# Kernel tuning notes

Hardware: AMD Instinct MI355X
Metric: run time of the kernel (lower is better)

Reference implementation:

```python
import jax, jax.numpy as jnp
import numpy as np

V = 96103   # pegasus-xsum vocab
D = 1024    # d_model
H = 16      # heads
DH = D // H
F = 4096    # ffn
L = 2       # enc and dec layers (reduced from 16 for the reference)
S = 512     # source length
T = 80      # max_length
B = 4       # batch of sources
NS = 5      # num_return_sequences
BN = B * NS # decode streams
TOPK = 100
EOS = 1
MINLEN = 7
EMB_SCALE = float(np.sqrt(D))


def ln(x):
    m = jnp.mean(x, -1, keepdims=True)
    v = jnp.mean((x - m) ** 2, -1, keepdims=True)
    return (x - m) * jax.lax.rsqrt(v + 1e-5)


def setup_inputs() -> dict:
    key = jax.random.key(0)
    ks = jax.random.split(key, 16)
    g = lambda k, s: (jax.random.normal(k, s) * 0.02).astype(jnp.float32)
    return {
        "ids": jax.random.randint(ks[0], (B, S), 0, 96000).astype(jnp.int32),
        "mask": jnp.ones((B, S), jnp.int32),
        "E": g(ks[1], (V, D)),
        "pos_e": g(ks[2], (S, D)),
        "pos_d": g(ks[3], (T, D)),
        "enc_attn_in": g(ks[4], (L, D, 3 * D)),
        "enc_attn_out": g(ks[5], (L, D, D)),
        "enc_ffn1": g(ks[6], (L, D, F)),
        "enc_ffn2": g(ks[7], (L, F, D)),
        "dec_sa_in": g(ks[8], (L, D, 3 * D)),
        "dec_sa_out": g(ks[9], (L, D, D)),
        "dec_ca_q": g(ks[10], (L, D, D)),
        "dec_ca_kv": g(ks[11], (L, D, 2 * D)),
        "dec_ca_out": g(ks[12], (L, D, D)),
        "dec_ffn1": g(ks[13], (L, D, F)),
        "dec_ffn2": g(ks[14], (L, F, D)),
    }


def _generate(ids, mask, E, pos_e, pos_d, enc_attn_in, enc_attn_out, enc_ffn1,
              enc_ffn2, dec_sa_in, dec_sa_out, dec_ca_q, dec_ca_kv, dec_ca_out,
              dec_ffn1, dec_ffn2):
    inv = 1.0 / float(np.sqrt(DH))
    # ---------------- encoder ----------------
    x = E[ids] * EMB_SCALE + pos_e[None]                       # [B,S,D]
    bias = (1.0 - mask.astype(jnp.float32))[:, None, None, :] * -1e9  # [B,1,1,S]
    for l in range(L):
        h = ln(x)
        qkv = h @ enc_attn_in[l]
        q = qkv[..., :D].reshape(B, S, H, DH)
        k = qkv[..., D:2 * D].reshape(B, S, H, DH)
        v = qkv[..., 2 * D:].reshape(B, S, H, DH)
        sc = jnp.einsum('bqhd,bkhd->bhqk', q, k) * inv + bias
        a = jnp.einsum('bhqk,bkhd->bqhd', jax.nn.softmax(sc, -1), v).reshape(B, S, D)
        x = x + a @ enc_attn_out[l]
        h = ln(x)
        x = x + jax.nn.gelu(h @ enc_ffn1[l]) @ enc_ffn2[l]
    enc = ln(x)
    # expand to BN = B * num_return_sequences decode streams
    enc_r = jnp.repeat(enc, NS, axis=0)                        # [BN,S,D]
    bias_r = jnp.repeat(bias, NS, axis=0)[:, :, 0, :]          # [BN,1,S]
    # precompute cross-attn K/V per decoder layer
    ckv = jnp.einsum('bsd,lde->lbse', enc_r, dec_ca_kv)        # [L,BN,S,2D]
    cK = ckv[..., :D].reshape(L, BN, S, H, DH)
    cV = ckv[..., D:].reshape(L, BN, S, H, DH)

    key_base = jax.random.key(1234)
    cache_k0 = jnp.zeros((L, BN, T, H, DH), jnp.float32)
    cache_v0 = jnp.zeros((L, BN, T, H, DH), jnp.float32)

    def step(carry, t):
        ck, cv, prev = carry
        x = E[prev] * EMB_SCALE + pos_d[t]                     # [BN,D]
        for l in range(L):
            h = ln(x)
            qkv = h @ dec_sa_in[l]
            q = qkv[:, :D].reshape(BN, H, DH)
            k = qkv[:, D:2 * D].reshape(BN, H, DH)
            v = qkv[:, 2 * D:].reshape(BN, H, DH)
            ck = ck.at[l, :, t].set(k)
            cv = cv.at[l, :, t].set(v)
            sc = jnp.einsum('bhd,bkhd->bhk', q, ck[l]) * inv
            sc = sc + jnp.where(jnp.arange(T) <= t, 0.0, -1e9)
            a = jnp.einsum('bhk,bkhd->bhd', jax.nn.softmax(sc, -1), cv[l]).reshape(BN, D)
            x = x + a @ dec_sa_out[l]
            h = ln(x)
            q2 = (h @ dec_ca_q[l]).reshape(BN, H, DH)
            sc2 = jnp.einsum('bhd,bshd->bhs', q2, cK[l]) * inv + bias_r
            a2 = jnp.einsum('bhs,bshd->bhd', jax.nn.softmax(sc2, -1), cV[l]).reshape(BN, D)
            x = x + a2 @ dec_ca_out[l]
            h = ln(x)
            x = x + jax.nn.gelu(h @ dec_ffn1[l]) @ dec_ffn2[l]
        x = ln(x)
        logits = x @ E.T                                       # [BN,V]
        forbid = (t < MINLEN - 1) & (jnp.arange(V) == EOS)     # min_length: block EOS
        logits = jnp.where(forbid, -1e9, logits)
        topv, topi = jax.lax.top_k(logits, TOPK)               # top_k=100 sampling
        sel = jax.random.categorical(jax.random.fold_in(key_base, t), topv)
        tok = jnp.take_along_axis(topi, sel[:, None], 1)[:, 0]
        lp = jnp.take_along_axis(jax.nn.log_softmax(logits, -1), tok[:, None], 1)[:, 0]
        return (ck, cv, tok), (tok, lp)

    init = (cache_k0, cache_v0, jnp.zeros((BN,), jnp.int32))  # start token = pad(0)
    _, (toks, lps) = jax.lax.scan(step, init, jnp.arange(T))
    return toks.T, lps.T                                       # [BN,T] each


def reference(ids, mask, E, pos_e, pos_d, enc_attn_in, enc_attn_out, enc_ffn1,
              enc_ffn2, dec_sa_in, dec_sa_out, dec_ca_q, dec_ca_kv, dec_ca_out,
              dec_ffn1, dec_ffn2):
    toks, _ = _generate(ids, mask, E, pos_e, pos_d, enc_attn_in, enc_attn_out,
                        enc_ffn1, enc_ffn2, dec_sa_in, dec_sa_out, dec_ca_q,
                        dec_ca_kv, dec_ca_out, dec_ffn1, dec_ffn2)
    # matches the torch module: [batch, num_seq, max_len] token ids
    return toks.reshape(B, NS, T)
```

## Files before the change

kernel.cpp:

```cpp
#include <hip/hip_runtime.h>
#include <cstdint>
#include <cstddef>

#define DEV __device__ __forceinline__

constexpr int V  = 96103;
constexpr int VPAD = 96104;
constexpr int D  = 1024;
constexpr int H  = 16;
constexpr int DH = 64;
constexpr int F  = 4096;
constexpr int NL = 2;
constexpr int S  = 512;
constexpr int T  = 80;
constexpr int B  = 4;
constexpr int NS = 5;
constexpr int BN = 20;
constexpr int KTOP = 100;
constexpr int EOS = 1;
constexpr int LCOLS = 188;
constexpr int LGRID = (V + LCOLS - 1) / LCOLS;


DEV float gelu_f(float x) {
  float x3 = x * x * x;
  float inner = 0.7978845608028654f * (x + 0.044715f * x3);
  float tt = tanhf(inner);
  return x * (0.5f * (1.0f + tt));
}

DEV void tf2x32(unsigned k0, unsigned k1, unsigned& x0, unsigned& x1) {
  unsigned ks2 = k0 ^ k1 ^ 0x1BD11BDAu;
#define TFR(rr) { x0 += x1; x1 = (x1 << rr) | (x1 >> (32 - rr)); x1 ^= x0; }
  x0 += k0; x1 += k1;
  TFR(13) TFR(15) TFR(26) TFR(6)
  x0 += k1;  x1 += ks2 + 1u;
  TFR(17) TFR(29) TFR(16) TFR(24)
  x0 += ks2; x1 += k0 + 2u;
  TFR(13) TFR(15) TFR(26) TFR(6)
  x0 += k0;  x1 += k1 + 3u;
  TFR(17) TFR(29) TFR(16) TFR(24)
  x0 += k1;  x1 += ks2 + 4u;
  TFR(13) TFR(15) TFR(26) TFR(6)
  x0 += ks2; x1 += k0 + 5u;
#undef TFR
}

DEV unsigned long long sort_key(float v, unsigned idx) {
  unsigned bb = __float_as_uint(v);
  bb = (bb & 0x80000000u) ? ~bb : (bb | 0x80000000u);
  return ((unsigned long long)bb << 32) | (unsigned long long)(0xFFFFFFFFu - idx);
}

template<int NWAVE>
DEV void ln_to_lds(const float* __restrict__ x, float* xs, int tid) {
  int w = tid >> 6, lane = tid & 63;
  for (int m = w; m < BN; m += NWAVE) {
    float4 v[4];
    float sum = 0.0f;
#pragma unroll
    for (int j = 0; j < 4; ++j) {
      v[j] = *(const float4*)(x + m * D + j * 256 + lane * 4);
      sum += v[j].x + v[j].y + v[j].z + v[j].w;
    }
#pragma unroll
    for (int o = 32; o > 0; o >>= 1) sum += __shfl_xor(sum, o);
    float mean = sum * (1.0f / 1024.0f);
    float vs = 0.0f;
#pragma unroll
    for (int j = 0; j < 4; ++j) {
      float a = v[j].x - mean, b = v[j].y - mean, c = v[j].z - mean, d = v[j].w - mean;
      vs += a * a + b * b + c * c + d * d;
    }
#pragma unroll
    for (int o = 32; o > 0; o >>= 1) vs += __shfl_xor(vs, o);
    float rsig = 1.0f / sqrtf(vs * (1.0f / 1024.0f) + 1e-5f);
#pragma unroll
    for (int j = 0; j < 4; ++j) {
      float4 ov;
      ov.x = (v[j].x - mean) * rsig; ov.y = (v[j].y - mean) * rsig;
      ov.z = (v[j].z - mean) * rsig; ov.w = (v[j].w - mean) * rsig;
      *(float4*)(xs + m * D + j * 256 + lane * 4) = ov;
    }
  }
}

DEV void row_ln_stats(const float* __restrict__ xd, int bn, float* xrow,
                      float* wred, float& rstd, float& bco, int tid) {
  int w = tid >> 6, lane = tid & 63;
  float4 v = *(const float4*)(xd + (size_t)bn * D + w * 256 + lane * 4);
  *(float4*)(xrow + w * 256 + lane * 4) = v;
  float s = v.x + v.y + v.z + v.w;
#pragma unroll
  for (int o = 32; o > 0; o >>= 1) s += __shfl_xor(s, o);
  if (lane == 0) wred[w] = s;
  __syncthreads();
  float mean = (wred[0] + wred[1] + wred[2] + wred[3]) * (1.0f / 1024.0f);
  float a = v.x - mean, b = v.y - mean, c = v.z - mean, d = v.w - mean;
  float s2 = a * a + b * b + c * c + d * d;
#pragma unroll
  for (int o = 32; o > 0; o >>= 1) s2 += __shfl_xor(s2, o);
  if (lane == 0) wred[4 + w] = s2;
  __syncthreads();
  rstd = 1.0f / sqrtf((wred[4] + wred[5] + wred[6] + wred[7]) * (1.0f / 1024.0f) + 1e-5f);
  bco = -mean * rstd;
}


__global__ __launch_bounds__(256) void embed_enc(const int* __restrict__ ids,
                                                 const float* __restrict__ E,
                                                 const float* __restrict__ pos_e,
                                                 float* __restrict__ xe) {
  int row = blockIdx.x;
  int id = ids[row];
  const float* er = E + (size_t)id * D;
  const float* pr = pos_e + (size_t)(row % S) * D;
  float* xr = xe + (size_t)row * D;
  for (int j = threadIdx.x; j < D; j += 256)
    xr[j] = er[j] * 32.0f + pr[j];
}

__global__ __launch_bounds__(256) void embed_dec(const float* __restrict__ E,
                                                 const float* __restrict__ pos_d,
                                                 const int* __restrict__ toks,
                                                 float* __restrict__ xd, int t) {
  int bn = blockIdx.x;
  int prev = (t == 0) ? 0 : toks[bn * T + (t - 1)];
  const float* er = E + (size_t)prev * D;
  const float* pr = pos_d + (size_t)t * D;
  float* xr = xd + (size_t)bn * D;
  for (int j = threadIdx.x; j < D; j += 256)
    xr[j] = er[j] * 32.0f + pr[j];
}


__global__ __launch_bounds__(256) void ln_kernel(const float* __restrict__ x,
                                                 float* __restrict__ y) {
  __shared__ float red[256];
  __shared__ float sv[2];
  int tid = threadIdx.x;
  const float* xr = x + (size_t)blockIdx.x * D;
  float4 v = *(const float4*)(xr + tid * 4);
  red[tid] = v.x + v.y + v.z + v.w;
  __syncthreads();
  for (int k = 128; k > 0; k >>= 1) { if (tid < k) red[tid] += red[tid + k]; __syncthreads(); }
  if (tid == 0) sv[0] = red[0] * (1.0f / 1024.0f);
  __syncthreads();
  float m = sv[0];
  float dx = v.x - m, dy = v.y - m, dz = v.z - m, dw = v.w - m;
  red[tid] = dx * dx + dy * dy + dz * dz + dw * dw;
  __syncthreads();
  for (int k = 128; k > 0; k >>= 1) { if (tid < k) red[tid] += red[tid + k]; __syncthreads(); }
  if (tid == 0) sv[1] = 1.0f / sqrtf(red[0] * (1.0f / 1024.0f) + 1e-5f);
  __syncthreads();
  float r = sv[1];
  float* yr = y + (size_t)blockIdx.x * D;
  float4 o; o.x = dx * r; o.y = dy * r; o.z = dz * r; o.w = dw * r;
  *(float4*)(yr + tid * 4) = o;
}


template<int EPI>
__global__ __launch_bounds__(256) void gemm128(const float* __restrict__ A,
                                               const float* __restrict__ W,
                                               const float* X, float* C,
                                               int Kd, int Nd) {
  __shared__ __align__(16) float As[8][128];
  __shared__ __align__(16) float Bs[8][128];
  int tid = threadIdx.x;
  int n0 = blockIdx.x * 128, m0 = blockIdx.y * 128;
  int tx = tid & 15, ty = tid >> 4;
  int ar = tid >> 1, ac = (tid & 1) * 4;
  int br = tid >> 5, bc = (tid & 31) * 4;
  float acc[8][8] = {};
  for (int k0 = 0; k0 < Kd; k0 += 8) {
    float4 av = *(const float4*)(A + (size_t)(m0 + ar) * Kd + k0 + ac);
    float4 wv = *(const float4*)(W + (size_t)(k0 + br) * Nd + n0 + bc);
    __syncthreads();
    As[ac + 0][ar] = av.x; As[ac + 1][ar] = av.y;
    As[ac + 2][ar] = av.z; As[ac + 3][ar] = av.w;
    *(float4*)&Bs[br][bc] = wv;
    __syncthreads();
#pragma unroll
    for (int k = 0; k < 8; ++k) {
      float a8[8], b8[8];
      *(float4*)&a8[0] = *(const float4*)&As[k][ty * 8];
      *(float4*)&a8[4] = *(const float4*)&As[k][ty * 8 + 4];
      *(float4*)&b8[0] = *(const float4*)&Bs[k][tx * 8];
      *(float4*)&b8[4] = *(const float4*)&Bs[k][tx * 8 + 4];
#pragma unroll
      for (int i = 0; i < 8; ++i)
#pragma unroll
        for (int j = 0; j < 8; ++j)
          acc[i][j] = fmaf(a8[i], b8[j], acc[i][j]);
    }
  }
#pragma unroll
  for (int i = 0; i < 8; ++i) {
    int m = m0 + ty * 8 + i;
#pragma unroll
    for (int j = 0; j < 8; ++j) {
      int n = n0 + tx * 8 + j;
      float r = acc[i][j];
      size_t off = (size_t)m * Nd + n;
      if (EPI == 1) r = X[off] + r;
      if (EPI == 2) r = gelu_f(r);
      C[off] = r;
    }
  }
}


__global__ __launch_bounds__(256) void enc_attn(const float* __restrict__ qkv,
                                                const int* __restrict__ mask,
                                                float* __restrict__ ab) {
  __shared__ __align__(16) float qv[64];
  __shared__ float sc[512];
  __shared__ float red[256];
  __shared__ float sv[2];
  int tid = threadIdx.x;
  int q = blockIdx.x % S;
  int h = (blockIdx.x / S) % H;
  int b = blockIdx.x / (S * H);
  const float* qrow = qkv + (size_t)(b * S + q) * (3 * D) + h * 64;
  if (tid < 64) qv[tid] = qrow[tid];
  __syncthreads();
  float lmax = -INFINITY;
  for (int k = tid; k < S; k += 256) {
    const float* kr = qkv + (size_t)(b * S + k) * (3 * D) + D + h * 64;
    float dot = 0.0f;
#pragma unroll
    for (int d4 = 0; d4 < 16; ++d4) {
      float4 kk = *(const float4*)(kr + d4 * 4);
      float4 qq = *(const float4*)(qv + d4 * 4);
      dot += qq.x * kk.x + qq.y * kk.y + qq.z * kk.z + qq.w * kk.w;
    }
    float bias = (1.0f - (float)mask[b * S + k]) * -1e9f;
    float val = dot * 0.125f + bias;
    sc[k] = val;
    lmax = fmaxf(lmax, val);
  }
  red[tid] = lmax; __syncthreads();
  for (int k = 128; k > 0; k >>= 1) { if (tid < k) red[tid] = fmaxf(red[tid], red[tid + k]); __syncthreads(); }
  if (tid == 0) sv[0] = red[0];
  __syncthreads();
  float mx = sv[0];
  float lsum = 0.0f;
  for (int k = tid; k < S; k += 256) { float e = expf(sc[k] - mx); sc[k] = e; lsum += e; }
  red[tid] = lsum; __syncthreads();
  for (int k = 128; k > 0; k >>= 1) { if (tid < k) red[tid] += red[tid + k]; __syncthreads(); }
  if (tid == 0) sv[1] = red[0];
  __syncthreads();
  float den = sv[1];
  for (int k = tid; k < S; k += 256) sc[k] = sc[k] / den;
  __syncthreads();
  int d = tid & 63, c = tid >> 6;
  const float* vb = qkv + (size_t)(b * S) * (3 * D) + 2 * D + h * 64 + d;
  float part = 0.0f;
  for (int k = c * 128; k < c * 128 + 128; ++k)
    part = fmaf(sc[k], vb[(size_t)k * (3 * D)], part);
  red[tid] = part; __syncthreads();
  if (tid < 64) {
    float o = red[tid] + red[tid + 64] + red[tid + 128] + red[tid + 192];
    ab[(size_t)(b * S + q) * D + h * 64 + tid] = o;
  }
}


template<int CT, int EPI, bool KV, bool LNIN>
__global__ __launch_bounds__(512) void dec_gemm(const float* __restrict__ x,
                                                const float* __restrict__ W,
                                                const float* Xres, float* Cout,
                                                float* __restrict__ cacheK,
                                                float* __restrict__ cacheV,
                                                int Kd, int Nd, int t, int l) {
  constexpr int KSP = 512 / CT;
  __shared__ float red[CT * 20 * (KSP + 1)];
  __shared__ float redw[CT * (KSP + 1)];
  __shared__ float sab[40];
  int tid = threadIdx.x;
  if constexpr (LNIN) {
    int w = tid >> 6, lane = tid & 63;
    for (int m = w; m < BN; m += 8) {
      const float* xr = x + (size_t)m * 1024 + lane * 16;
      float4 v[4];
      float sum = 0.0f;
#pragma unroll
      for (int j = 0; j < 4; ++j) {
        v[j] = *(const float4*)(xr + j * 4);
        sum += v[j].x + v[j].y + v[j].z + v[j].w;
      }
#pragma unroll
      for (int o = 32; o > 0; o >>= 1) sum += __shfl_xor(sum, o);
      float mean = sum * (1.0f / 1024.0f);
      float vs = 0.0f;
#pragma unroll
      for (int j = 0; j < 4; ++j) {
        float a = v[j].x - mean, b = v[j].y - mean, c2 = v[j].z - mean, d = v[j].w - mean;
        vs += a * a + b * b + c2 * c2 + d * d;
      }
#pragma unroll
      for (int o = 32; o > 0; o >>= 1) vs += __shfl_xor(vs, o);
      float rstd = 1.0f / sqrtf(vs * (1.0f / 1024.0f) + 1e-5f);
      if (lane == 0) { sab[m] = rstd; sab[20 + m] = -mean * rstd; }
    }
    __syncthreads();
  }
  int c = tid % CT, ks = tid / CT;
  int klen = Kd / KSP;
  const float* Wp = W + (size_t)(ks * klen) * Nd + blockIdx.x * CT + c;
  float acc[20] = {};
  float accw = 0.0f;
  for (int kk = 0; kk < klen; kk += 8) {
    float wv[8];
#pragma unroll
    for (int u = 0; u < 8; ++u) wv[u] = Wp[(size_t)u * Nd];
    Wp += (size_t)8 * Nd;
    if constexpr (LNIN)
      accw += wv[0] + wv[1] + wv[2] + wv[3] + wv[4] + wv[5] + wv[6] + wv[7];
    int kb = ks * klen + kk;
#pragma unroll
    for (int m = 0; m < 20; ++m) {
      float4 x0 = *(const float4*)(x + (size_t)m * Kd + kb);
      float4 x1 = *(const float4*)(x + (size_t)m * Kd + kb + 4);
      float a = acc[m];
      a = fmaf(x0.x, wv[0], a); a = fmaf(x0.y, wv[1], a);
      a = fmaf(x0.z, wv[2], a); a = fmaf(x0.w, wv[3], a);
      a = fmaf(x1.x, wv[4], a); a = fmaf(x1.y, wv[5], a);
      a = fmaf(x1.z, wv[6], a); a = fmaf(x1.w, wv[7], a);
      acc[m] = a;
    }
  }
#pragma unroll
  for (int m = 0; m < 20; ++m) red[(c * 20 + m) * (KSP + 1) + ks] = acc[m];
  if constexpr (LNIN) redw[c * (KSP + 1) + ks] = accw;
  __syncthreads();
  if (tid < CT * 20) {
    int cc = tid % CT, m = tid / CT;
    const float* rp = red + (cc * 20 + m) * (KSP + 1);
    float s = 0.0f;
#pragma unroll
    for (int k2 = 0; k2 < KSP; ++k2) s += rp[k2];
    if constexpr (LNIN) {
      const float* rw = redw + cc * (KSP + 1);
      float sw = 0.0f;
#pragma unroll
      for (int k2 = 0; k2 < KSP; ++k2) sw += rw[k2];
      s = sab[m] * s + sab[20 + m] * sw;
    }
    int ng = blockIdx.x * CT + cc;
    if constexpr (KV) {
      if (ng < D) {
        Cout[(size_t)m * Nd + ng] = s;
      } else if (ng < 2 * D) {
        cacheK[(((size_t)l * BN + m) * T + t) * D + (ng - D)] = s;
      } else {
        cacheV[(((size_t)l * BN + m) * T + t) * D + (ng - 2 * D)] = s;
      }
    } else {
      size_t off = (size_t)m * Nd + ng;
      if (EPI == 1) s = Xres[off] + s;
      if (EPI == 2) s = gelu_f(s);
      Cout[off] = s;
    }
  }
}


__global__ __launch_bounds__(256) void qkv_selfattn(const float* __restrict__ xd,
                                                    const float* __restrict__ Wqkv,
                                                    float* __restrict__ cacheK,
                                                    float* __restrict__ cacheV,
                                                    float* __restrict__ ad,
                                                    int t, int l) {
  __shared__ __align__(16) float xrow[1024];
  __shared__ __align__(16) float qv[64], kt[64], vt[64];
  __shared__ float sc[96];
  __shared__ float wred[8];
  __shared__ float sv[2];
  int tid = threadIdx.x;
  int h = blockIdx.x / BN, bn = blockIdx.x % BN;
  float rstd, bco;
  row_ln_stats(xd, bn, xrow, wred, rstd, bco, tid);
  __syncthreads();
  if (tid < 192) {
    int part = tid >> 6;
    int c = tid & 63;
    const float* Wp = Wqkv + (size_t)part * D + (size_t)h * 64 + c;
    float acc = 0.0f, accw = 0.0f;
    for (int k = 0; k < 1024; k += 8) {
      float wv[8];
#pragma unroll
      for (int u = 0; u < 8; ++u) wv[u] = Wp[(size_t)(k + u) * (3 * D)];
#pragma unroll
      for (int u = 0; u < 8; ++u) {
        acc = fmaf(xrow[k + u], wv[u], acc);
        accw += wv[u];
      }
    }
    float val = rstd * acc + bco * accw;
    if (part == 0) {
      qv[c] = val;
    } else if (part == 1) {
      kt[c] = val;
      cacheK[(((size_t)l * BN + bn) * T + t) * D + h * 64 + c] = val;
    } else {
      vt[c] = val;
      cacheV[(((size_t)l * BN + bn) * T + t) * D + h * 64 + c] = val;
    }
  }
  __syncthreads();
  int n = t + 1;
  if (tid < t) {
    const float* kr = cacheK + (((size_t)l * BN + bn) * T + tid) * D + h * 64;
    float dot = 0.0f;
#pragma unroll
    for (int d4 = 0; d4 < 16; ++d4) {
      float4 kk = *(const float4*)(kr + d4 * 4);
      float4 qq = *(const float4*)(qv + d4 * 4);
      dot += qq.x * kk.x + qq.y * kk.y + qq.z * kk.z + qq.w * kk.w;
    }
    sc[tid] = dot * 0.125f;
  } else if (tid == t) {
    float dot = 0.0f;
#pragma unroll
    for (int d4 = 0; d4 < 16; ++d4) {
      float4 kk = *(const float4*)(kt + d4 * 4);
      float4 qq = *(const float4*)(qv + d4 * 4);
      dot += qq.x * kk.x + qq.y * kk.y + qq.z * kk.z + qq.w * kk.w;
    }
    sc[t] = dot * 0.125f;
  }
  __syncthreads();
  if (tid == 0) {
    float mx = -INFINITY;
    for (int k = 0; k < n; ++k) mx = fmaxf(mx, sc[k]);
    sv[0] = mx;
  }
  __syncthreads();
  if (tid < n) sc[tid] = expf(sc[tid] - sv[0]);
  __syncthreads();
  if (tid == 0) {
    float s = 0.0f;
    for (int k = 0; k < n; ++k) s += sc[k];
    sv[1] = s;
  }
  __syncthreads();
  if (tid < n) sc[tid] = sc[tid] / sv[1];
  __syncthreads();
  if (tid < 64) {
    const float* vb = cacheV + ((size_t)l * BN + bn) * T * D + h * 64 + tid;
    float o = 0.0f;
    for (int k = 0; k < t; ++k) o = fmaf(sc[k], vb[(size_t)k * D], o);
    o = fmaf(sc[t], vt[tid], o);
    ad[(size_t)bn * D + h * 64 + tid] = o;
  }
}


__global__ __launch_bounds__(256) void caq_crossattn(const float* __restrict__ xd,
                                                     const float* __restrict__ Wcq,
                                                     const float* __restrict__ cKVl,
                                                     const int* __restrict__ mask,
                                                     float* __restrict__ ad) {
  __shared__ __align__(16) float xrow[1024];
  __shared__ __align__(16) float qv[64];
  __shared__ float sc[512];
  __shared__ float red[256];
  __shared__ float qred[256], qredw[256];
  __shared__ float wred[8];
  __shared__ float sv[2];
  int tid = threadIdx.x;
  int h = blockIdx.x / BN, bn = blockIdx.x % BN;
  int b = bn / NS;
  float rstd, bco;
  row_ln_stats(xd, bn, xrow, wred, rstd, bco, tid);
  __syncthreads();
  {
    int c = tid & 63, ks = tid >> 6;
    const float* Wp = Wcq + (size_t)(ks * 256) * D + (size_t)h * 64 + c;
    float acc = 0.0f, accw = 0.0f;
    for (int k = 0; k < 256; k += 8) {
      float wv[8];
#pragma unroll
      for (int u = 0; u < 8; ++u) wv[u] = Wp[(size_t)(k + u) * D];
#pragma unroll
      for (int u = 0; u < 8; ++u) {
        acc = fmaf(xrow[ks * 256 + k + u], wv[u], acc);
        accw += wv[u];
      }
    }
    qred[ks * 64 + c] = acc;
    qredw[ks * 64 + c] = accw;
  }
  __syncthreads();
  if (tid < 64) {
    float a = qred[tid] + qred[64 + tid] + qred[128 + tid] + qred[192 + tid];
    float aw = qredw[tid] + qredw[64 + tid] + qredw[128 + tid] + qredw[192 + tid];
    qv[tid] = rstd * a + bco * aw;
  }
  __syncthreads();
  const float* base = cKVl + (size_t)b * S * (2 * D);
  float lmax = -INFINITY;
  for (int s = tid; s < S; s += 256) {
    const float* kr = base + (size_t)s * (2 * D) + h * 64;
    float dot = 0.0f;
#pragma unroll
    for (int d4 = 0; d4 < 16; ++d4) {
      float4 kk = *(const float4*)(kr + d4 * 4);
      float4 qq = *(const float4*)(qv + d4 * 4);
      dot += qq.x * kk.x + qq.y * kk.y + qq.z * kk.z + qq.w * kk.w;
    }
    float bias = (1.0f - (float)mask[b * S + s]) * -1e9f;
    float val = dot * 0.125f + bias;
    sc[s] = val;
    lmax = fmaxf(lmax, val);
  }
  red[tid] = lmax; __syncthreads();
  for (int k = 128; k > 0; k >>= 1) { if (tid < k) red[tid] = fmaxf(red[tid], red[tid + k]); __syncthreads(); }
  if (tid == 0) sv[0] = red[0];
  __syncthreads();
  float mx = sv[0];
  float lsum = 0.0f;
  for (int s = tid; s < S; s += 256) { float e = expf(sc[s] - mx); sc[s] = e; lsum += e; }
  red[tid] = lsum; __syncthreads();
  for (int k = 128; k > 0; k >>= 1) { if (tid < k) red[tid] += red[tid + k]; __syncthreads(); }
  if (tid == 0) sv[1] = red[0];
  __syncthreads();
  float den = sv[1];
  for (int s = tid; s < S; s += 256) sc[s] = sc[s] / den;
  __syncthreads();
  int d = tid & 63, c = tid >> 6;
  const float* vb = base + D + h * 64 + d;
  float part = 0.0f;
  for (int s = c * 128; s < c * 128 + 128; ++s)
    part = fmaf(sc[s], vb[(size_t)s * (2 * D)], part);
  red[tid] = part; __syncthreads();
  if (tid < 64) {
    float o = red[tid] + red[tid + 64] + red[tid + 128] + red[tid + 192];
    ad[(size_t)bn * D + h * 64 + tid] = o;
  }
}


__global__ __launch_bounds__(256) void logits3(const float* __restrict__ xd,
                                               const float* __restrict__ E,
                                               float* __restrict__ logits) {
  __shared__ float xs[20 * 1024];
  int tid = threadIdx.x;
  ln_to_lds<4>(xd, xs, tid);
  __syncthreads();
  int n = blockIdx.x * LCOLS + tid;
  if (tid < LCOLS && n < V) {
    const float* er = E + (size_t)n * D;
    float acc[20] = {};
    for (int k = 0; k < 1024; k += 8) {
      float4 e0 = *(const float4*)(er + k);
      float4 e1 = *(const float4*)(er + k + 4);
#pragma unroll
      for (int m = 0; m < 20; ++m) {
        const float* xb = xs + m * 1024 + k;
        float4 x0 = *(const float4*)(xb);
        float4 x1 = *(const float4*)(xb + 4);
        float a = acc[m];
        a = fmaf(x0.x, e0.x, a); a = fmaf(x0.y, e0.y, a);
        a = fmaf(x0.z, e0.z, a); a = fmaf(x0.w, e0.w, a);
        a = fmaf(x1.x, e1.x, a); a = fmaf(x1.y, e1.y, a);
        a = fmaf(x1.z, e1.z, a); a = fmaf(x1.w, e1.w, a);
        acc[m] = a;
      }
    }
#pragma unroll
    for (int m = 0; m < 20; ++m)
      logits[(size_t)m * VPAD + n] = acc[m];
  } else if (n == V) {
#pragma unroll
    for (int m = 0; m < 20; ++m)
      logits[(size_t)m * VPAD + V] = -1e30f;
  }
}


__global__ __launch_bounds__(256) void topk_sample(const float* __restrict__ logits,
                                                   int* __restrict__ toks,
                                                   const float* __restrict__ E,
                                                   const float* __restrict__ pos_d,
                                                   float* __restrict__ xd, int t) {
  __shared__ unsigned long long keys[2048];
  __shared__ float svals[128];
  __shared__ unsigned sidx[128];
  __shared__ int stok;
  int tid = threadIdx.x;
  int bn = blockIdx.x;
  const float* row = logits + (size_t)bn * VPAD;

  float tv[8]; unsigned ti[8];
#pragma unroll
  for (int j = 0; j < 8; ++j) { tv[j] = -INFINITY; ti[j] = 0xFFFFFFFFu; }

  for (int i4 = tid * 4; i4 < VPAD; i4 += 1024) {
    float4 v4 = *(const float4*)(row + i4);
    float vv[4] = {v4.x, v4.y, v4.z, v4.w};
#pragma unroll
    for (int j = 0; j < 4; ++j) {
      int i = i4 + j;
      float v = vv[j];
      if (t < 6 && i == EOS) v = -1e9f;
      if (v > tv[7]) {
        tv[7] = v; ti[7] = (unsigned)i;
#pragma unroll
        for (int jj = 7; jj > 0; --jj) {
          if (tv[jj] > tv[jj - 1]) {
            float a = tv[jj]; tv[jj] = tv[jj - 1]; tv[jj - 1] = a;
            unsigned bi = ti[jj]; ti[jj] = ti[jj - 1]; ti[jj - 1] = bi;
          }
        }
      }
    }
  }
#pragma unroll
  for (int j = 0; j < 8; ++j) keys[tid * 8 + j] = ~sort_key(tv[j], ti[j]);
  __syncthreads();

  for (int ksz = 2; ksz <= 2048; ksz <<= 1) {
    for (int jj = ksz >> 1; jj > 0; jj >>= 1) {
      for (int i = tid; i < 2048; i += 256) {
        int ixj = i ^ jj;
        if (ixj > i) {
          unsigned long long a = keys[i], b2 = keys[ixj];
          bool up = ((i & ksz) == 0);
          if ((a > b2) == up) { keys[i] = b2; keys[ixj] = a; }
        }
      }
      __syncthreads();
    }
  }

  if (tid < KTOP) {
    unsigned long long kk = ~keys[tid];
    unsigned sb = (unsigned)(kk >> 32);
    unsigned idx = 0xFFFFFFFFu - (unsigned)(kk & 0xFFFFFFFFull);
    unsigned fb = (sb & 0x80000000u) ? (sb ^ 0x80000000u) : ~sb;
    float v = __uint_as_float(fb);
    unsigned a0 = 0u, a1 = (unsigned)t;
    tf2x32(0u, 1234u, a0, a1);
    unsigned c0 = 0u, c1 = (unsigned)(bn * KTOP + tid);
    tf2x32(a0, a1, c0, c1);
    unsigned bits = c0 ^ c1;
    float f = __uint_as_float((bits >> 9) | 0x3f800000u) - 1.0f;
    float u = fmaxf(f, 1.17549435e-38f);
    float g = -logf(-logf(u));
    svals[tid] = v + g;
    sidx[tid] = idx;
  }
  __syncthreads();
  if (tid == 0) {
    int best = 0; float bv = svals[0];
    for (int j = 1; j < KTOP; ++j) { if (svals[j] > bv) { bv = svals[j]; best = j; } }
    int tok = (int)sidx[best];
    toks[bn * T + t] = tok;
    stok = tok;
  }
  __syncthreads();
  if (t + 1 < T) {
    int tok = stok;
    const float* er = E + (size_t)tok * D;
    const float* pr = pos_d + (size_t)(t + 1) * D;
    for (int j = tid; j < D; j += 256)
      xd[(size_t)bn * D + j] = er[j] * 32.0f + pr[j];
  }
}


extern "C" void kernel_launch(void* const* d_in, const int* in_sizes, int n_in,
                              void* d_out, int out_size, void* d_ws, size_t ws_size,
                              hipStream_t stream) {
  (void)in_sizes; (void)n_in; (void)out_size; (void)ws_size;

  const int*   ids   = (const int*)d_in[0];
  const int*   maskp = (const int*)d_in[1];
  const float* E     = (const float*)d_in[2];
  const float* pos_e = (const float*)d_in[3];
  const float* pos_d = (const float*)d_in[4];
  const float* eai   = (const float*)d_in[5];
  const float* eao   = (const float*)d_in[6];
  const float* ef1   = (const float*)d_in[7];
  const float* ef2   = (const float*)d_in[8];
  const float* dsi   = (const float*)d_in[9];
  const float* dso   = (const float*)d_in[10];
  const float* dcq   = (const float*)d_in[11];
  const float* dckv  = (const float*)d_in[12];
  const float* dco   = (const float*)d_in[13];
  const float* df1   = (const float*)d_in[14];
  const float* df2   = (const float*)d_in[15];

  float* ws = (float*)d_ws;
  size_t o = 0;
  auto alloc = [&](size_t n) { size_t r = o; o += (n + 63) & ~(size_t)63; return r; };
  float* cKV    = ws + alloc((size_t)NL * B * S * 2 * D);
  float* cacheK = ws + alloc((size_t)NL * BN * T * D);
  float* cacheV = ws + alloc((size_t)NL * BN * T * D);
  float* xe     = ws + alloc((size_t)B * S * D);
  float* he     = ws + alloc((size_t)B * S * D);
  float* qkvb   = ws + alloc((size_t)B * S * 3 * D);
  float* ab     = ws + alloc((size_t)B * S * D);
  float* ffb    = ws + alloc((size_t)B * S * F);
  float* xd      = qkvb;
  float* q2      = xd + BN * D;
  float* ad      = q2 + BN * D;
  float* qkvd    = ad + BN * D;
  float* ffd     = qkvd + BN * 3 * D;
  float* logitsb = ffd + BN * F;
  int* toks = (int*)d_out;
  (void)q2; (void)qkvd;

  embed_enc<<<B * S, 256, 0, stream>>>(ids, E, pos_e, xe);
  for (int l = 0; l < NL; ++l) {
    ln_kernel<<<B * S, 256, 0, stream>>>(xe, he);
    gemm128<0><<<dim3(3 * D / 128, B * S / 128), 256, 0, stream>>>(
        he, eai + (size_t)l * D * 3 * D, nullptr, qkvb, D, 3 * D);
    enc_attn<<<B * H * S, 256, 0, stream>>>(qkvb, maskp, ab);
    gemm128<1><<<dim3(D / 128, B * S / 128), 256, 0, stream>>>(
        ab, eao + (size_t)l * D * D, xe, xe, D, D);
    ln_kernel<<<B * S, 256, 0, stream>>>(xe, he);
    gemm128<2><<<dim3(F / 128, B * S / 128), 256, 0, stream>>>(
        he, ef1 + (size_t)l * D * F, nullptr, ffb, D, F);
    gemm128<1><<<dim3(D / 128, B * S / 128), 256, 0, stream>>>(
        ffb, ef2 + (size_t)l * F * D, xe, xe, F, D);
  }
  ln_kernel<<<B * S, 256, 0, stream>>>(xe, he);
  for (int l = 0; l < NL; ++l) {
    gemm128<0><<<dim3(2 * D / 128, B * S / 128), 256, 0, stream>>>(
        he, dckv + (size_t)l * D * 2 * D, nullptr,
        cKV + (size_t)l * B * S * 2 * D, D, 2 * D);
  }

  embed_dec<<<BN, 256, 0, stream>>>(E, pos_d, toks, xd, 0);
  for (int t = 0; t < T; ++t) {
    for (int l = 0; l < NL; ++l) {
      qkv_selfattn<<<H * BN, 256, 0, stream>>>(
          xd, dsi + (size_t)l * D * 3 * D, cacheK, cacheV, ad, t, l);
      dec_gemm<8, 1, false, false><<<D / 8, 512, 0, stream>>>(
          ad, dso + (size_t)l * D * D, xd, xd, nullptr, nullptr, D, D, 0, 0);
      caq_crossattn<<<H * BN, 256, 0, stream>>>(
          xd, dcq + (size_t)l * D * D, cKV + (size_t)l * B * S * 2 * D, maskp, ad);
      dec_gemm<8, 1, false, false><<<D / 8, 512, 0, stream>>>(
          ad, dco + (size_t)l * D * D, xd, xd, nullptr, nullptr, D, D, 0, 0);
      dec_gemm<16, 2, false, true><<<F / 16, 512, 0, stream>>>(
          xd, df1 + (size_t)l * D * F, nullptr, ffd, nullptr, nullptr, D, F, 0, 0);
      dec_gemm<8, 1, false, false><<<D / 8, 512, 0, stream>>>(
          ffd, df2 + (size_t)l * F * D, xd, xd, nullptr, nullptr, F, D, 0, 0);
    }
    logits3<<<LGRID, 256, 0, stream>>>(xd, E, logitsb);
    topk_sample<<<BN, 256, 0, stream>>>(logitsb, toks, E, pos_d, xd, t);
  }
}
```

Measured before the change: 54.64 ms.

## Retile vocab logits kernel across warps and widen decoder GEMM column tiles

The logits kernel is restructured so each of the four 64-lane wavefronts handles 5 of the 20 decode rows and each lane computes 6 vocab columns. Previously a single thread covered all 20 rows for one column, with 188 active threads per block. The new mapping keeps all 256 threads busy and reuses each LDS-loaded x value across 6 embedding rows, which lowers LDS traffic per FMA. In exchange, each embedding row is now read by four wavefronts instead of one, increasing global/L2 reads of E. Separately, the small decoder GEMMs move from 8 to 16 columns per block, halving their grid size, and unused scratch buffers are dropped.

```diff
diff --git a/kernel.cpp b/kernel.cpp
--- a/kernel.cpp
+++ b/kernel.cpp
@@ -18,8 +18,9 @@
 constexpr int BN = 20;
 constexpr int KTOP = 100;
 constexpr int EOS = 1;
-constexpr int LCOLS = 188;
-constexpr int LGRID = (V + LCOLS - 1) / LCOLS;
+constexpr int L4C = 6;
+constexpr int L4COLS = 64 * L4C;
+constexpr int L4GRID = (V + L4COLS - 1) / L4COLS;
 
 
 DEV float gelu_f(float x) {
@@ -543,37 +544,54 @@
 }
 
 
-__global__ __launch_bounds__(256) void logits3(const float* __restrict__ xd,
+__global__ __launch_bounds__(256) void logits4(const float* __restrict__ xd,
                                                const float* __restrict__ E,
                                                float* __restrict__ logits) {
   __shared__ float xs[20 * 1024];
   int tid = threadIdx.x;
   ln_to_lds<4>(xd, xs, tid);
   __syncthreads();
-  int n = blockIdx.x * LCOLS + tid;
-  if (tid < LCOLS && n < V) {
-    const float* er = E + (size_t)n * D;
-    float acc[20] = {};
-    for (int k = 0; k < 1024; k += 8) {
-      float4 e0 = *(const float4*)(er + k);
-      float4 e1 = *(const float4*)(er + k + 4);
-#pragma unroll
-      for (int m = 0; m < 20; ++m) {
-        const float* xb = xs + m * 1024 + k;
-        float4 x0 = *(const float4*)(xb);
-        float4 x1 = *(const float4*)(xb + 4);
-        float a = acc[m];
-        a = fmaf(x0.x, e0.x, a); a = fmaf(x0.y, e0.y, a);
-        a = fmaf(x0.z, e0.z, a); a = fmaf(x0.w, e0.w, a);
-        a = fmaf(x1.x, e1.x, a); a = fmaf(x1.y, e1.y, a);
-        a = fmaf(x1.z, e1.z, a); a = fmaf(x1.w, e1.w, a);
-        acc[m] = a;
+  int w = tid >> 6, lane = tid & 63;
+  int mrow = w * 5;
+  int base = blockIdx.x * L4COLS + lane;
+  const float* er[L4C];
+  int nn[L4C];
+#pragma unroll
+  for (int j = 0; j < L4C; ++j) {
+    int n = base + j * 64;
+    nn[j] = n;
+    er[j] = E + (size_t)(n < V ? n : V - 1) * D;
+  }
+  float acc[5][L4C] = {};
+  for (int k = 0; k < 1024; k += 8) {
+    float4 e0[L4C], e1[L4C];
+#pragma unroll
+    for (int j = 0; j < L4C; ++j) {
+      e0[j] = *(const float4*)(er[j] + k);
+      e1[j] = *(const float4*)(er[j] + k + 4);
+    }
+#pragma unroll
+    for (int m = 0; m < 5; ++m) {
+      const float* xb = xs + (mrow + m) * 1024 + k;
+      float4 x0 = *(const float4*)xb;
+      float4 x1 = *(const float4*)(xb + 4);
+#pragma unroll
+      for (int j = 0; j < L4C; ++j) {
+        float a = acc[m][j];
+        a = fmaf(x0.x, e0[j].x, a); a = fmaf(x0.y, e0[j].y, a);
+        a = fmaf(x0.z, e0[j].z, a); a = fmaf(x0.w, e0[j].w, a);
+        a = fmaf(x1.x, e1[j].x, a); a = fmaf(x1.y, e1[j].y, a);
+        a = fmaf(x1.z, e1[j].z, a); a = fmaf(x1.w, e1[j].w, a);
+        acc[m][j] = a;
       }
     }
-#pragma unroll
-    for (int m = 0; m < 20; ++m)
-      logits[(size_t)m * VPAD + n] = acc[m];
-  } else if (n == V) {
+  }
+#pragma unroll
+  for (int m = 0; m < 5; ++m)
+#pragma unroll
+    for (int j = 0; j < L4C; ++j)
+      if (nn[j] < V) logits[(size_t)(mrow + m) * VPAD + nn[j]] = acc[m][j];
+  if (blockIdx.x == 0 && tid == 0) {
 #pragma unroll
     for (int m = 0; m < 20; ++m)
       logits[(size_t)m * VPAD + V] = -1e30f;
@@ -706,13 +724,10 @@
   float* ab     = ws + alloc((size_t)B * S * D);
   float* ffb    = ws + alloc((size_t)B * S * F);
   float* xd      = qkvb;
-  float* q2      = xd + BN * D;
-  float* ad      = q2 + BN * D;
-  float* qkvd    = ad + BN * D;
-  float* ffd     = qkvd + BN * 3 * D;
+  float* ad      = xd + BN * D;
+  float* ffd     = ad + BN * D;
   float* logitsb = ffd + BN * F;
   int* toks = (int*)d_out;
-  (void)q2; (void)qkvd;
 
   embed_enc<<<B * S, 256, 0, stream>>>(ids, E, pos_e, xe);
   for (int l = 0; l < NL; ++l) {
@@ -740,18 +755,18 @@
     for (int l = 0; l < NL; ++l) {
       qkv_selfattn<<<H * BN, 256, 0, stream>>>(
           xd, dsi + (size_t)l * D * 3 * D, cacheK, cacheV, ad, t, l);
-      dec_gemm<8, 1, false, false><<<D / 8, 512, 0, stream>>>(
+      dec_gemm<16, 1, false, false><<<D / 16, 512, 0, stream>>>(
           ad, dso + (size_t)l * D * D, xd, xd, nullptr, nullptr, D, D, 0, 0);
       caq_crossattn<<<H * BN, 256, 0, stream>>>(
           xd, dcq + (size_t)l * D * D, cKV + (size_t)l * B * S * 2 * D, maskp, ad);
-      dec_gemm<8, 1, false, false><<<D / 8, 512, 0, stream>>>(
+      dec_gemm<16, 1, false, false><<<D / 16, 512, 0, stream>>>(
           ad, dco + (size_t)l * D * D, xd, xd, nullptr, nullptr, D, D, 0, 0);
       dec_gemm<16, 2, false, true><<<F / 16, 512, 0, stream>>>(
           xd, df1 + (size_t)l * D * F, nullptr, ffd, nullptr, nullptr, D, F, 0, 0);
-      dec_gemm<8, 1, false, false><<<D / 8, 512, 0, stream>>>(
+      dec_gemm<16, 1, false, false><<<D / 16, 512, 0, stream>>>(
           ffd, df2 + (size_t)l * F * D, xd, xd, nullptr, nullptr, F, D, 0, 0);
     }
-    logits3<<<LGRID, 256, 0, stream>>>(xd, E, logitsb);
+    logits4<<<L4GRID, 256, 0, stream>>>(xd, E, logitsb);
     topk_sample<<<BN, 256, 0, stream>>>(logitsb, toks, E, pos_d, xd, t);
   }
 }
```

Result: slower. 66.49 ms (+21.7%).

## Fuse self-attention output projection into attention kernel and residual sum into cross-attention

Applied to the files above, without the earlier changes.

Each self-attention block now multiplies its 64-wide head output by its slice of the output projection and writes per-head partial rows. The cross-attention kernel sums those 16 partials with the residual, recomputes the layernorm stats in registers, and the head-0 block writes the new residual. This removes one dec_gemm launch per layer per decode step, at the cost of redundant partial-sum reads in every cross-attention block and an extra 16x partial buffer.

```diff
diff --git a/kernel.cpp b/kernel.cpp
--- a/kernel.cpp
+++ b/kernel.cpp
@@ -367,14 +367,15 @@
 }
 
 
-__global__ __launch_bounds__(256) void qkv_selfattn(const float* __restrict__ xd,
-                                                    const float* __restrict__ Wqkv,
-                                                    float* __restrict__ cacheK,
-                                                    float* __restrict__ cacheV,
-                                                    float* __restrict__ ad,
-                                                    int t, int l) {
+__global__ __launch_bounds__(256) void qkv_selfattn2(const float* __restrict__ xd,
+                                                     const float* __restrict__ Wqkv,
+                                                     const float* __restrict__ Wso,
+                                                     float* __restrict__ cacheK,
+                                                     float* __restrict__ cacheV,
+                                                     float* __restrict__ part1,
+                                                     int t, int l) {
   __shared__ __align__(16) float xrow[1024];
-  __shared__ __align__(16) float qv[64], kt[64], vt[64];
+  __shared__ __align__(16) float qv[64], kt[64], vt[64], ov[64];
   __shared__ float sc[96];
   __shared__ float wred[8];
   __shared__ float sv[2];
@@ -453,16 +454,31 @@
     float o = 0.0f;
     for (int k = 0; k < t; ++k) o = fmaf(sc[k], vb[(size_t)k * D], o);
     o = fmaf(sc[t], vt[tid], o);
-    ad[(size_t)bn * D + h * 64 + tid] = o;
-  }
-}
-
-
-__global__ __launch_bounds__(256) void caq_crossattn(const float* __restrict__ xd,
-                                                     const float* __restrict__ Wcq,
-                                                     const float* __restrict__ cKVl,
-                                                     const int* __restrict__ mask,
-                                                     float* __restrict__ ad) {
+    ov[tid] = o;
+  }
+  __syncthreads();
+  {
+    int c0 = tid * 4;
+    const float* wbase = Wso + (size_t)(h * 64) * D + c0;
+    float4 a = {0.0f, 0.0f, 0.0f, 0.0f};
+    for (int j = 0; j < 64; ++j) {
+      float oj = ov[j];
+      float4 wr = *(const float4*)(wbase + (size_t)j * D);
+      a.x = fmaf(oj, wr.x, a.x); a.y = fmaf(oj, wr.y, a.y);
+      a.z = fmaf(oj, wr.z, a.z); a.w = fmaf(oj, wr.w, a.w);
+    }
+    *(float4*)(part1 + ((size_t)h * BN + bn) * D + c0) = a;
+  }
+}
+
+
+__global__ __launch_bounds__(256) void caq_crossattn2(const float* __restrict__ xd,
+                                                      const float* __restrict__ part1,
+                                                      const float* __restrict__ Wcq,
+                                                      const float* __restrict__ cKVl,
+                                                      const int* __restrict__ mask,
+                                                      float* __restrict__ y,
+                                                      float* __restrict__ ad) {
   __shared__ __align__(16) float xrow[1024];
   __shared__ __align__(16) float qv[64];
   __shared__ float sc[512];
@@ -473,9 +489,29 @@
   int tid = threadIdx.x;
   int h = blockIdx.x / BN, bn = blockIdx.x % BN;
   int b = bn / NS;
-  float rstd, bco;
-  row_ln_stats(xd, bn, xrow, wred, rstd, bco, tid);
-  __syncthreads();
+  int w = tid >> 6, lane = tid & 63;
+  int c0 = tid * 4;
+  float4 r = *(const float4*)(xd + (size_t)bn * D + c0);
+  for (int hh = 0; hh < H; ++hh) {
+    float4 p = *(const float4*)(part1 + ((size_t)hh * BN + bn) * D + c0);
+    r.x += p.x; r.y += p.y; r.z += p.z; r.w += p.w;
+  }
+  *(float4*)(xrow + c0) = r;
+  if (h == 0) *(float4*)(y + (size_t)bn * D + c0) = r;
+  float s = r.x + r.y + r.z + r.w;
+#pragma unroll
+  for (int o = 32; o > 0; o >>= 1) s += __shfl_xor(s, o);
+  if (lane == 0) wred[w] = s;
+  __syncthreads();
+  float mean = (wred[0] + wred[1] + wred[2] + wred[3]) * (1.0f / 1024.0f);
+  float da = r.x - mean, db = r.y - mean, dc = r.z - mean, dd = r.w - mean;
+  float s2 = da * da + db * db + dc * dc + dd * dd;
+#pragma unroll
+  for (int o = 32; o > 0; o >>= 1) s2 += __shfl_xor(s2, o);
+  if (lane == 0) wred[4 + w] = s2;
+  __syncthreads();
+  float rstd = 1.0f / sqrtf((wred[4] + wred[5] + wred[6] + wred[7]) * (1.0f / 1024.0f) + 1e-5f);
+  float bco = -mean * rstd;
   {
     int c = tid & 63, ks = tid >> 6;
     const float* Wp = Wcq + (size_t)(ks * 256) * D + (size_t)h * 64 + c;
@@ -502,8 +538,8 @@
   __syncthreads();
   const float* base = cKVl + (size_t)b * S * (2 * D);
   float lmax = -INFINITY;
-  for (int s = tid; s < S; s += 256) {
-    const float* kr = base + (size_t)s * (2 * D) + h * 64;
+  for (int s3 = tid; s3 < S; s3 += 256) {
+    const float* kr = base + (size_t)s3 * (2 * D) + h * 64;
     float dot = 0.0f;
 #pragma unroll
     for (int d4 = 0; d4 < 16; ++d4) {
@@ -511,9 +547,9 @@
       float4 qq = *(const float4*)(qv + d4 * 4);
       dot += qq.x * kk.x + qq.y * kk.y + qq.z * kk.z + qq.w * kk.w;
     }
-    float bias = (1.0f - (float)mask[b * S + s]) * -1e9f;
+    float bias = (1.0f - (float)mask[b * S + s3]) * -1e9f;
     float val = dot * 0.125f + bias;
-    sc[s] = val;
+    sc[s3] = val;
     lmax = fmaxf(lmax, val);
   }
   red[tid] = lmax; __syncthreads();
@@ -522,19 +558,19 @@
   __syncthreads();
   float mx = sv[0];
   float lsum = 0.0f;
-  for (int s = tid; s < S; s += 256) { float e = expf(sc[s] - mx); sc[s] = e; lsum += e; }
+  for (int s3 = tid; s3 < S; s3 += 256) { float e = expf(sc[s3] - mx); sc[s3] = e; lsum += e; }
   red[tid] = lsum; __syncthreads();
   for (int k = 128; k > 0; k >>= 1) { if (tid < k) red[tid] += red[tid + k]; __syncthreads(); }
   if (tid == 0) sv[1] = red[0];
   __syncthreads();
   float den = sv[1];
-  for (int s = tid; s < S; s += 256) sc[s] = sc[s] / den;
+  for (int s3 = tid; s3 < S; s3 += 256) sc[s3] = sc[s3] / den;
   __syncthreads();
   int d = tid & 63, c = tid >> 6;
   const float* vb = base + D + h * 64 + d;
   float part = 0.0f;
-  for (int s = c * 128; s < c * 128 + 128; ++s)
-    part = fmaf(sc[s], vb[(size_t)s * (2 * D)], part);
+  for (int s3 = c * 128; s3 < c * 128 + 128; ++s3)
+    part = fmaf(sc[s3], vb[(size_t)s3 * (2 * D)], part);
   red[tid] = part; __syncthreads();
   if (tid < 64) {
     float o = red[tid] + red[tid + 64] + red[tid + 128] + red[tid + 192];
@@ -706,13 +742,13 @@
   float* ab     = ws + alloc((size_t)B * S * D);
   float* ffb    = ws + alloc((size_t)B * S * F);
   float* xd      = qkvb;
-  float* q2      = xd + BN * D;
-  float* ad      = q2 + BN * D;
-  float* qkvd    = ad + BN * D;
-  float* ffd     = qkvd + BN * 3 * D;
-  float* logitsb = ffd + BN * F;
+  float* ad      = xd + BN * D;
+  float* yb      = ad + BN * D;
+  float* y2b     = yb + BN * D;
+  float* ffd     = y2b + BN * D;
+  float* part1   = ffd + BN * F;
+  float* logitsb = part1 + H * BN * D;
   int* toks = (int*)d_out;
-  (void)q2; (void)qkvd;
 
   embed_enc<<<B * S, 256, 0, stream>>>(ids, E, pos_e, xe);
   for (int l = 0; l < NL; ++l) {
@@ -738,18 +774,18 @@
   embed_dec<<<BN, 256, 0, stream>>>(E, pos_d, toks, xd, 0);
   for (int t = 0; t < T; ++t) {
     for (int l = 0; l < NL; ++l) {
-      qkv_selfattn<<<H * BN, 256, 0, stream>>>(
-          xd, dsi + (size_t)l * D * 3 * D, cacheK, cacheV, ad, t, l);
+      qkv_selfattn2<<<H * BN, 256, 0, stream>>>(
+          xd, dsi + (size_t)l * D * 3 * D, dso + (size_t)l * D * D,
+          cacheK, cacheV, part1, t, l);
+      caq_crossattn2<<<H * BN, 256, 0, stream>>>(
+          xd, part1, dcq + (size_t)l * D * D,
+          cKV + (size_t)l * B * S * 2 * D, maskp, yb, ad);
       dec_gemm<8, 1, false, false><<<D / 8, 512, 0, stream>>>(
-          ad, dso + (size_t)l * D * D, xd, xd, nullptr, nullptr, D, D, 0, 0);
-      caq_crossattn<<<H * BN, 256, 0, stream>>>(
-          xd, dcq + (size_t)l * D * D, cKV + (size_t)l * B * S * 2 * D, maskp, ad);
+          ad, dco + (size_t)l * D * D, yb, y2b, nullptr, nullptr, D, D, 0, 0);
+      dec_gemm<16, 2, false, true><<<F / 16, 512, 0, stream>>>(
+          y2b, df1 + (size_t)l * D * F, nullptr, ffd, nullptr, nullptr, D, F, 0, 0);
       dec_gemm<8, 1, false, false><<<D / 8, 512, 0, stream>>>(
-          ad, dco + (size_t)l * D * D, xd, xd, nullptr, nullptr, D, D, 0, 0);
-      dec_gemm<16, 2, false, true><<<F / 16, 512, 0, stream>>>(
-          xd, df1 + (size_t)l * D * F, nullptr, ffd, nullptr, nullptr, D, F, 0, 0);
-      dec_gemm<8, 1, false, false><<<D / 8, 512, 0, stream>>>(
-          ffd, df2 + (size_t)l * F * D, xd, xd, nullptr, nullptr, F, D, 0, 0);
+          ffd, df2 + (size_t)l * F * D, y2b, xd, nullptr, nullptr, F, D, 0, 0);
     }
     logits3<<<LGRID, 256, 0, stream>>>(xd, E, logitsb);
     topk_sample<<<BN, 256, 0, stream>>>(logitsb, toks, E, pos_d, xd, t);
```

After: 54.09 ms. Within noise of the previous version (-1.0%).
